# Optimization experiments

Hardware: AMD Instinct MI355X
Metric: run time of the kernel (lower is better)

Reference implementation:

```python
import jax, jax.numpy as jnp
import numpy as np

N_SITES = 100000
DIM = 128
KSIZE = 7  # 7^3 = 343 offsets
GRID = 160


def _build_sparse_structure(seed=0):
    """Sample N_SITES unique voxels in a GRID^3 volume and build the
    depthwise-conv kernel map: neighbor_idx[i, k] = index of site at
    coords[i] + offset[k], or N_SITES (sentinel -> zero row) if absent."""
    rng = np.random.default_rng(seed)
    lin = rng.choice(GRID ** 3, size=N_SITES, replace=False)
    coords = np.stack(np.unravel_index(lin, (GRID, GRID, GRID)), axis=1).astype(np.int64)  # [N,3]
    lookup = np.full(GRID ** 3, N_SITES, dtype=np.int32)
    lookup[lin] = np.arange(N_SITES, dtype=np.int32)
    r = KSIZE // 2
    offs = np.stack(np.meshgrid(*([np.arange(-r, r + 1)] * 3), indexing="ij"), axis=-1).reshape(-1, 3)  # [343,3]
    K = offs.shape[0]
    neighbor_idx = np.full((N_SITES, K), N_SITES, dtype=np.int32)
    for k in range(K):
        nb = coords + offs[k]
        ok = np.all((nb >= 0) & (nb < GRID), axis=1)
        nb_lin = (nb[ok, 0] * GRID + nb[ok, 1]) * GRID + nb[ok, 2]
        neighbor_idx[ok, k] = lookup[nb_lin]
    return neighbor_idx


def setup_inputs() -> dict:
    key = jax.random.key(0)
    ks = jax.random.split(key, 12)
    neighbor_idx = jnp.asarray(_build_sparse_structure(0))
    d, h = DIM, 4 * DIM
    K = KSIZE ** 3
    return {
        "feats": jax.random.normal(ks[0], (N_SITES, d), jnp.float32),
        "neighbor_idx": neighbor_idx,
        "dw_w": jax.random.normal(ks[1], (K, d), jnp.float32) * 0.05,
        "dw_b": jax.random.normal(ks[2], (d,), jnp.float32) * 0.02,
        "ln_g": 1.0 + 0.1 * jax.random.normal(ks[3], (d,), jnp.float32),
        "ln_b": 0.02 * jax.random.normal(ks[4], (d,), jnp.float32),
        "w1": jax.random.normal(ks[5], (d, h), jnp.float32) * (1.0 / np.sqrt(d)),
        "b1": 0.02 * jax.random.normal(ks[6], (h,), jnp.float32),
        "grn_g": 0.1 * jax.random.normal(ks[7], (1, h), jnp.float32),
        "grn_b": 0.02 * jax.random.normal(ks[8], (1, h), jnp.float32),
        "w2": jax.random.normal(ks[9], (h, d), jnp.float32) * (1.0 / np.sqrt(h)),
        "b2": 0.02 * jax.random.normal(ks[10], (d,), jnp.float32),
    }


def reference(feats, neighbor_idx, dw_w, dw_b, ln_g, ln_b, w1, b1, grn_g, grn_b, w2, b2):
    eps = 1e-6
    n, d = feats.shape
    # --- sparse depthwise conv: gather-multiply-accumulate over kernel offsets ---
    f_pad = jnp.concatenate([feats, jnp.zeros((1, d), feats.dtype)], axis=0)  # sentinel row

    def step(acc, xs):
        idx_k, w_k = xs  # idx_k: [N], w_k: [dim]
        return acc + f_pad[idx_k] * w_k, None

    x, _ = jax.lax.scan(step, jnp.zeros_like(feats), (neighbor_idx.T, dw_w))
    x = x + dw_b
    # --- LayerNorm over channels ---
    mu = jnp.mean(x, axis=-1, keepdims=True)
    var = jnp.var(x, axis=-1, keepdims=True)
    x = (x - mu) / jnp.sqrt(var + eps) * ln_g + ln_b
    # --- pwconv1 -> GELU (exact, matching torch default) ---
    x = jax.nn.gelu(x @ w1 + b1, approximate=False)  # [N, 4*dim]
    # --- GRN: L2 norm over all sites (dim=0), per channel ---
    gx = jnp.sqrt(jnp.sum(x * x, axis=0, keepdims=True))  # [1, 4*dim]
    nx = gx / (jnp.mean(gx, axis=-1, keepdims=True) + eps)
    x = grn_g * (x * nx) + grn_b + x
    # --- pwconv2 + residual (drop_path identity in eval) ---
    x = x @ w2 + b2
    return feats + x
```

## Files before the change

### kernel.cpp

```cpp
#include <hip/hip_runtime.h>

typedef unsigned short u16;
typedef unsigned int u32;
typedef __attribute__((ext_vector_type(8))) short bf16x8;
typedef __attribute__((ext_vector_type(4))) float f32x4;

__device__ __forceinline__ u16 f2bf(float f) {
    u32 u = __float_as_uint(f);
    return (u16)((u + 0x7FFFu + ((u >> 16) & 1u)) >> 16);
}
__device__ __forceinline__ int sw_idx(int r, int c) { return r * 16 + (c ^ (r & 15)); }

__device__ __forceinline__ float fast_gelu(float x) {
    const float x3 = x * x * x;
    const float y2 = 1.5957691216057308f * (x + 0.044715f * x3);
    const float u = __expf(fminf(y2, 80.f));
    const float th = (u - 1.f) / (u + 1.f);
    return 0.5f * x * (1.f + th);
}

__global__ __launch_bounds__(256) void cast_feats_k(
    const float* __restrict__ src, u16* __restrict__ dst, int n4)
{
    const int e = blockIdx.x * 256 + threadIdx.x;
    if (e >= n4) return;
    const float4 v = *(const float4*)(src + (size_t)e * 4);
    uint2 o;
    o.x = (u32)f2bf(v.x) | ((u32)f2bf(v.y) << 16);
    o.y = (u32)f2bf(v.z) | ((u32)f2bf(v.w) << 16);
    *(uint2*)(dst + (size_t)e * 4) = o;
}

__global__ __launch_bounds__(256) void dwln_k(
    const u16* __restrict__ featsb, const int* __restrict__ nb,
    const u16* __restrict__ dwwb, const float* __restrict__ dw_b,
    const float* __restrict__ ln_g, const float* __restrict__ ln_b,
    u16* __restrict__ xln, int nsites)
{
    __shared__ int lists[8][348];
    const int w = threadIdx.x >> 6;
    const int lane = threadIdx.x & 63;
    const int s0 = blockIdx.x * 8 + w * 2;
    if (s0 >= nsites) return;
    const bool two = (s0 + 1) < nsites;
    const int* rowA = nb + (size_t)s0 * 343;
    const int* rowB = nb + (size_t)(two ? s0 + 1 : s0) * 343;
    int idxA[6], idxB[6];
    #pragma unroll
    for (int j = 0; j < 5; ++j) {
        idxA[j] = rowA[lane + j * 64];
        const int vb = rowB[lane + j * 64];
        idxB[j] = two ? vb : nsites;
    }
    idxA[5] = (lane < 23) ? rowA[320 + lane] : nsites;
    idxB[5] = (two && lane < 23) ? rowB[320 + lane] : nsites;
    int cA = 0, cB = 0;
    #pragma unroll
    for (int i = 0; i < 6; ++i) {
        cA += (idxA[i] < nsites) ? 1 : 0;
        cB += (idxB[i] < nsites) ? 1 : 0;
    }
    const int packed = cA | (cB << 16);
    int pre = packed;
    #pragma unroll
    for (int off = 1; off < 64; off <<= 1) {
        const int v = __shfl_up(pre, off, 64);
        if (lane >= off) pre += v;
    }
    const int tot = __shfl(pre, 63, 64);
    const int cntA = tot & 0xFFFF, cntB = tot >> 16;
    pre -= packed;
    int pA = pre & 0xFFFF, pB = pre >> 16;
    #pragma unroll
    for (int i = 0; i < 6; ++i) {
        const int k = (i < 5) ? (lane + i * 64) : (320 + lane);
        if (idxA[i] < nsites) lists[w * 2][pA++] = idxA[i] | (k << 17);
        if (idxB[i] < nsites) lists[w * 2 + 1][pB++] = idxB[i] | (k << 17);
    }
    float xA0 = 0.f, xA1 = 0.f, xB0 = 0.f, xB1 = 0.f;
    const int mx = (cntA > cntB) ? cntA : cntB;
    for (int base = 0; base < mx; base += 4) {
        u32 fa[4], wa[4], fb[4], wb[4];
        #pragma unroll
        for (int i = 0; i < 4; ++i) {
            if (base + i < cntA) {
                const int p = lists[w * 2][base + i];
                fa[i] = *(const u32*)(featsb + (size_t)(p & 0x1FFFF) * 128 + lane * 2);
                wa[i] = *(const u32*)(dwwb + (size_t)(p >> 17) * 128 + lane * 2);
            } else { fa[i] = 0u; wa[i] = 0u; }
            if (base + i < cntB) {
                const int p = lists[w * 2 + 1][base + i];
                fb[i] = *(const u32*)(featsb + (size_t)(p & 0x1FFFF) * 128 + lane * 2);
                wb[i] = *(const u32*)(dwwb + (size_t)(p >> 17) * 128 + lane * 2);
            } else { fb[i] = 0u; wb[i] = 0u; }
        }
        #pragma unroll
        for (int i = 0; i < 4; ++i) {
            xA0 += __uint_as_float(fa[i] << 16) * __uint_as_float(wa[i] << 16);
            xA1 += __uint_as_float(fa[i] & 0xFFFF0000u) * __uint_as_float(wa[i] & 0xFFFF0000u);
            xB0 += __uint_as_float(fb[i] << 16) * __uint_as_float(wb[i] << 16);
            xB1 += __uint_as_float(fb[i] & 0xFFFF0000u) * __uint_as_float(wb[i] & 0xFFFF0000u);
        }
    }
    const float2 bv = *(const float2*)(dw_b + lane * 2);
    const float2 gv = *(const float2*)(ln_g + lane * 2);
    const float2 lbv = *(const float2*)(ln_b + lane * 2);
    #pragma unroll
    for (int sidx = 0; sidx < 2; ++sidx) {
        if (sidx == 1 && !two) break;
        float a0 = (sidx == 0) ? xA0 : xB0;
        float a1 = (sidx == 0) ? xA1 : xB1;
        a0 += bv.x; a1 += bv.y;
        float s = a0 + a1, ss = a0 * a0 + a1 * a1;
        #pragma unroll
        for (int off = 32; off > 0; off >>= 1) {
            s += __shfl_xor(s, off, 64);
            ss += __shfl_xor(ss, off, 64);
        }
        const float mean = s * (1.f / 128.f);
        const float var = ss * (1.f / 128.f) - mean * mean;
        const float rstd = rsqrtf(fmaxf(var, 0.f) + 1e-6f);
        const float y0 = (a0 - mean) * rstd * gv.x + lbv.x;
        const float y1 = (a1 - mean) * rstd * gv.y + lbv.y;
        *(u32*)(xln + (size_t)(s0 + sidx) * 128 + lane * 2) =
            (u32)f2bf(y0) | ((u32)f2bf(y1) << 16);
    }
}

__global__ __launch_bounds__(256) void transpose_w1_k(
    const float* __restrict__ w1, u16* __restrict__ w1t)
{
    const int e = blockIdx.x * 256 + threadIdx.x;
    const int n = e >> 7, k = e & 127;
    w1t[e] = f2bf(w1[k * 512 + n]);
}

__global__ __launch_bounds__(256, 4) void gemm1_k(
    const u16* __restrict__ xln, const u16* __restrict__ w1t,
    const float* __restrict__ b1, u16* __restrict__ h,
    float* __restrict__ gx_sq, int nsites)
{
    __shared__ float s_red[128];
    const int t = threadIdx.x;
    const int n0 = blockIdx.x * 128;
    const int m0 = blockIdx.y * 64;
    const int lane = t & 63;
    const int w = t >> 6;
    const int wn = w * 32;
    const int l15 = lane & 15, quad = lane >> 4;
    if (t < 128) s_red[t] = 0.f;
    __syncthreads();
    f32x4 acc[2][4];
    #pragma unroll
    for (int i = 0; i < 2; ++i)
        #pragma unroll
        for (int j = 0; j < 4; ++j) acc[i][j] = f32x4{0.f, 0.f, 0.f, 0.f};
    const u16* a_base = w1t + (size_t)(n0 + wn + l15) * 128 + quad * 8;
    const u16* b_base = xln + (size_t)(m0 + l15) * 128 + quad * 8;
    #pragma unroll
    for (int ks = 0; ks < 4; ++ks) {
        const int koff = ks * 32;
        bf16x8 a[2], b[4];
        #pragma unroll
        for (int nt = 0; nt < 2; ++nt)
            a[nt] = *(const bf16x8*)(a_base + (size_t)nt * 16 * 128 + koff);
        #pragma unroll
        for (int mt = 0; mt < 4; ++mt)
            b[mt] = *(const bf16x8*)(b_base + (size_t)mt * 16 * 128 + koff);
        #pragma unroll
        for (int nt = 0; nt < 2; ++nt)
            #pragma unroll
            for (int mt = 0; mt < 4; ++mt)
                acc[nt][mt] = __builtin_amdgcn_mfma_f32_16x16x32_bf16(a[nt], b[mt], acc[nt][mt], 0, 0, 0);
    }
    float ssl[2][4] = {{0.f,0.f,0.f,0.f},{0.f,0.f,0.f,0.f}};
    #pragma unroll
    for (int nt = 0; nt < 2; ++nt) {
        const int chb = n0 + wn + nt * 16 + quad * 4;
        const float4 b1v = *(const float4*)(b1 + chb);
        #pragma unroll
        for (int mt = 0; mt < 4; ++mt) {
            const int site = m0 + mt * 16 + l15;
            if (site < nsites) {
                float v[4];
                #pragma unroll
                for (int rg = 0; rg < 4; ++rg) {
                    v[rg] = fast_gelu(acc[nt][mt][rg] + ((const float*)&b1v)[rg]);
                    ssl[nt][rg] += v[rg] * v[rg];
                }
                uint2 o;
                o.x = (u32)f2bf(v[0]) | ((u32)f2bf(v[1]) << 16);
                o.y = (u32)f2bf(v[2]) | ((u32)f2bf(v[3]) << 16);
                *(uint2*)(h + (size_t)site * 512 + chb) = o;
            }
        }
    }
    #pragma unroll
    for (int nt = 0; nt < 2; ++nt)
        #pragma unroll
        for (int rg = 0; rg < 4; ++rg) {
            float v = ssl[nt][rg];
            v += __shfl_xor(v, 1, 64);
            v += __shfl_xor(v, 2, 64);
            v += __shfl_xor(v, 4, 64);
            v += __shfl_xor(v, 8, 64);
            if (l15 == 0) atomicAdd(&s_red[wn + nt * 16 + quad * 4 + rg], v);
        }
    __syncthreads();
    if (t < 128) atomicAdd(&gx_sq[n0 + t], s_red[t]);
}

__global__ __launch_bounds__(512) void grn_scale_k(
    const float* __restrict__ gx_sq, const float* __restrict__ grn_g,
    const float* __restrict__ grn_b, const float* __restrict__ w2,
    const float* __restrict__ b2, float* __restrict__ scale, float* __restrict__ b_eff)
{
    __shared__ float red[512];
    __shared__ float redb[512];
    const int t = threadIdx.x;
    const float g = sqrtf(gx_sq[t]);
    red[t] = g;
    __syncthreads();
    #pragma unroll
    for (int off = 256; off > 0; off >>= 1) {
        if (t < off) red[t] += red[t + off];
        __syncthreads();
    }
    const float mean = red[0] * (1.f / 512.f);
    scale[t] = grn_g[t] * (g / (mean + 1e-6f)) + 1.f;
    const int dc = t & 127, grp = t >> 7;
    float p = 0.f;
    #pragma unroll 8
    for (int i = 0; i < 128; ++i) {
        const int c = grp * 128 + i;
        p += grn_b[c] * w2[(size_t)c * 128 + dc];
    }
    redb[t] = p;
    __syncthreads();
    if (t < 128) b_eff[t] = b2[t] + redb[t] + redb[t + 128] + redb[t + 256] + redb[t + 384];
}

__global__ __launch_bounds__(256) void w2t_k(
    const float* __restrict__ scale, const float* __restrict__ w2,
    u16* __restrict__ w2t)
{
    const int e = blockIdx.x * 256 + threadIdx.x;
    const int c = e & 511, dc = e >> 9;
    w2t[e] = f2bf(scale[c] * w2[(size_t)c * 128 + dc]);
}

__global__ __launch_bounds__(256, 4) void gemm2_k(
    const u16* __restrict__ h, const u16* __restrict__ w2t,
    const float* __restrict__ b_eff, const float* __restrict__ feats,
    float* __restrict__ out, int nsites)
{
    const int t = threadIdx.x;
    const int m0 = blockIdx.x * 64;
    const int lane = t & 63;
    const int w = t >> 6;
    const int wn = w * 32;
    const int l15 = lane & 15, quad = lane >> 4;
    f32x4 acc[4][2];
    #pragma unroll
    for (int i = 0; i < 4; ++i)
        #pragma unroll
        for (int j = 0; j < 2; ++j) acc[i][j] = f32x4{0.f, 0.f, 0.f, 0.f};
    const u16* a_base = h + (size_t)(m0 + l15) * 512 + quad * 8;
    const u16* b_base = w2t + (size_t)(wn + l15) * 512 + quad * 8;
    #pragma unroll
    for (int ks = 0; ks < 16; ++ks) {
        const int koff = ks * 32;
        bf16x8 a[4], b[2];
        #pragma unroll
        for (int mt = 0; mt < 4; ++mt)
            a[mt] = *(const bf16x8*)(a_base + (size_t)mt * 16 * 512 + koff);
        #pragma unroll
        for (int nt = 0; nt < 2; ++nt)
            b[nt] = *(const bf16x8*)(b_base + (size_t)nt * 16 * 512 + koff);
        #pragma unroll
        for (int mt = 0; mt < 4; ++mt)
            #pragma unroll
            for (int nt = 0; nt < 2; ++nt)
                acc[mt][nt] = __builtin_amdgcn_mfma_f32_16x16x32_bf16(a[mt], b[nt], acc[mt][nt], 0, 0, 0);
    }
    float be[2]; int col[2];
    #pragma unroll
    for (int nt = 0; nt < 2; ++nt) {
        col[nt] = wn + nt * 16 + l15;
        be[nt] = b_eff[col[nt]];
    }
    #pragma unroll
    for (int mt = 0; mt < 4; ++mt) {
        const int rbase = m0 + mt * 16 + quad * 4;
        #pragma unroll
        for (int nt = 0; nt < 2; ++nt) {
            #pragma unroll
            for (int rg = 0; rg < 4; ++rg) {
                const int rowg = rbase + rg;
                if (rowg < nsites) {
                    out[(size_t)rowg * 128 + col[nt]] =
                        acc[mt][nt][rg] + be[nt] + feats[(size_t)rowg * 128 + col[nt]];
                }
            }
        }
    }
}

extern "C" void kernel_launch(void* const* d_in, const int* in_sizes, int n_in,
                              void* d_out, int out_size, void* d_ws, size_t ws_size,
                              hipStream_t stream) {
    const float* feats = (const float*)d_in[0];
    const int* nb      = (const int*)d_in[1];
    const float* dw_w  = (const float*)d_in[2];
    const float* dw_b  = (const float*)d_in[3];
    const float* ln_g  = (const float*)d_in[4];
    const float* ln_b  = (const float*)d_in[5];
    const float* w1    = (const float*)d_in[6];
    const float* b1    = (const float*)d_in[7];
    const float* grn_g = (const float*)d_in[8];
    const float* grn_b = (const float*)d_in[9];
    const float* w2    = (const float*)d_in[10];
    const float* b2    = (const float*)d_in[11];
    float* out = (float*)d_out;
    const int nsites = in_sizes[0] / 128;

    char* ws = (char*)d_ws;
    size_t off = 0;
    u16* xln   = (u16*)(ws + off);  off += (((size_t)(nsites + 128) * 128 * 2) + 255) & ~(size_t)255;
    u16* h     = (u16*)(ws + off);  off += (((size_t)(nsites + 128) * 512 * 2) + 255) & ~(size_t)255;
    u16* featsb= (u16*)(ws + off);  off += (((size_t)nsites * 128 * 2) + 255) & ~(size_t)255;
    u16* dwwb  = (u16*)(ws + off);  off += 343 * 128 * 2 + 128;
    u16* w1t   = (u16*)(ws + off);  off += 512 * 128 * 2;
    u16* w2t   = (u16*)(ws + off);  off += 128 * 512 * 2;
    float* gx_sq = (float*)(ws + off); off += 512 * 4;
    float* scale = (float*)(ws + off); off += 512 * 4;
    float* b_eff = (float*)(ws + off); off += 128 * 4;

    hipMemsetAsync(gx_sq, 0, 512 * sizeof(float), stream);
    const int nfeat4 = nsites * 32;
    cast_feats_k<<<(nfeat4 + 255) / 256, 256, 0, stream>>>(feats, featsb, nfeat4);
    const int ndww4 = 343 * 32;
    cast_feats_k<<<(ndww4 + 255) / 256, 256, 0, stream>>>(dw_w, dwwb, ndww4);
    transpose_w1_k<<<256, 256, 0, stream>>>(w1, w1t);
    dwln_k<<<(nsites + 7) / 8, 256, 0, stream>>>(featsb, nb, dwwb, dw_b, ln_g, ln_b, xln, nsites);
    const int m1blocks = (nsites + 63) / 64;
    gemm1_k<<<dim3(4, m1blocks), 256, 0, stream>>>(xln, w1t, b1, h, gx_sq, nsites);
    grn_scale_k<<<1, 512, 0, stream>>>(gx_sq, grn_g, grn_b, w2, b2, scale, b_eff);
    w2t_k<<<256, 256, 0, stream>>>(scale, w2, w2t);
    const int m2blocks = (nsites + 63) / 64;
    gemm2_k<<<m2blocks, 256, 0, stream>>>(h, w2t, b_eff, feats, out, nsites);
}
```

Baseline: 491.0 us.

## Prefetch next K-slice in GEMMs, vectorize gemm2 epilogue, split b_eff reduction

Both MFMA GEMM kernels now double-buffer their register operands, loading the next K-slice before issuing the current MFMAs so global-load latency overlaps compute. gemm2 swaps its operand roles so each lane owns four consecutive output channels, which lets the epilogue read feats and write out with float4 accesses instead of scalar ones. The grn_b·w2 bias reduction moves out of the single-block GRN kernel into a separate 8-block kernel that uses atomics and runs before the conv. This shortens the serial tail between the GEMMs, at the cost of an extra memset, atomics and more register pressure.

```diff
diff --git a/kernel.cpp b/kernel.cpp
--- a/kernel.cpp
+++ b/kernel.cpp
@@ -9,7 +9,6 @@
     u32 u = __float_as_uint(f);
     return (u16)((u + 0x7FFFu + ((u >> 16) & 1u)) >> 16);
 }
-__device__ __forceinline__ int sw_idx(int r, int c) { return r * 16 + (c ^ (r & 15)); }
 
 __device__ __forceinline__ float fast_gelu(float x) {
     const float x3 = x * x * x;
@@ -157,21 +156,33 @@
         for (int j = 0; j < 4; ++j) acc[i][j] = f32x4{0.f, 0.f, 0.f, 0.f};
     const u16* a_base = w1t + (size_t)(n0 + wn + l15) * 128 + quad * 8;
     const u16* b_base = xln + (size_t)(m0 + l15) * 128 + quad * 8;
+    bf16x8 aC[2], bC[4], aN[2], bN[4];
+    #pragma unroll
+    for (int nt = 0; nt < 2; ++nt) aC[nt] = *(const bf16x8*)(a_base + (size_t)nt * 16 * 128);
+    #pragma unroll
+    for (int mt = 0; mt < 4; ++mt) bC[mt] = *(const bf16x8*)(b_base + (size_t)mt * 16 * 128);
     #pragma unroll
     for (int ks = 0; ks < 4; ++ks) {
-        const int koff = ks * 32;
-        bf16x8 a[2], b[4];
+        if (ks < 3) {
+            const int koff = (ks + 1) * 32;
+            #pragma unroll
+            for (int nt = 0; nt < 2; ++nt)
+                aN[nt] = *(const bf16x8*)(a_base + (size_t)nt * 16 * 128 + koff);
+            #pragma unroll
+            for (int mt = 0; mt < 4; ++mt)
+                bN[mt] = *(const bf16x8*)(b_base + (size_t)mt * 16 * 128 + koff);
+        }
         #pragma unroll
         for (int nt = 0; nt < 2; ++nt)
-            a[nt] = *(const bf16x8*)(a_base + (size_t)nt * 16 * 128 + koff);
-        #pragma unroll
-        for (int mt = 0; mt < 4; ++mt)
-            b[mt] = *(const bf16x8*)(b_base + (size_t)mt * 16 * 128 + koff);
-        #pragma unroll
-        for (int nt = 0; nt < 2; ++nt)
             #pragma unroll
             for (int mt = 0; mt < 4; ++mt)
-                acc[nt][mt] = __builtin_amdgcn_mfma_f32_16x16x32_bf16(a[nt], b[mt], acc[nt][mt], 0, 0, 0);
+                acc[nt][mt] = __builtin_amdgcn_mfma_f32_16x16x32_bf16(aC[nt], bC[mt], acc[nt][mt], 0, 0, 0);
+        if (ks < 3) {
+            #pragma unroll
+            for (int nt = 0; nt < 2; ++nt) aC[nt] = aN[nt];
+            #pragma unroll
+            for (int mt = 0; mt < 4; ++mt) bC[mt] = bN[mt];
+        }
     }
     float ssl[2][4] = {{0.f,0.f,0.f,0.f},{0.f,0.f,0.f,0.f}};
     #pragma unroll
@@ -210,13 +221,30 @@
     if (t < 128) atomicAdd(&gx_sq[n0 + t], s_red[t]);
 }
 
+__global__ __launch_bounds__(256) void beff_k(
+    const float* __restrict__ grn_b, const float* __restrict__ w2,
+    float* __restrict__ b_eff)
+{
+    __shared__ float red[256];
+    const int t = threadIdx.x;
+    const int dc = t & 127, part = t >> 7;
+    const int c0 = blockIdx.x * 64 + part * 32;
+    float p = 0.f;
+    #pragma unroll 8
+    for (int i = 0; i < 32; ++i) {
+        const int c = c0 + i;
+        p += grn_b[c] * w2[(size_t)c * 128 + dc];
+    }
+    red[t] = p;
+    __syncthreads();
+    if (t < 128) atomicAdd(&b_eff[t], red[t] + red[t + 128]);
+}
+
 __global__ __launch_bounds__(512) void grn_scale_k(
     const float* __restrict__ gx_sq, const float* __restrict__ grn_g,
-    const float* __restrict__ grn_b, const float* __restrict__ w2,
-    const float* __restrict__ b2, float* __restrict__ scale, float* __restrict__ b_eff)
+    float* __restrict__ scale)
 {
     __shared__ float red[512];
-    __shared__ float redb[512];
     const int t = threadIdx.x;
     const float g = sqrtf(gx_sq[t]);
     red[t] = g;
@@ -228,16 +256,6 @@
     }
     const float mean = red[0] * (1.f / 512.f);
     scale[t] = grn_g[t] * (g / (mean + 1e-6f)) + 1.f;
-    const int dc = t & 127, grp = t >> 7;
-    float p = 0.f;
-    #pragma unroll 8
-    for (int i = 0; i < 128; ++i) {
-        const int c = grp * 128 + i;
-        p += grn_b[c] * w2[(size_t)c * 128 + dc];
-    }
-    redb[t] = p;
-    __syncthreads();
-    if (t < 128) b_eff[t] = b2[t] + redb[t] + redb[t + 128] + redb[t + 256] + redb[t + 384];
 }
 
 __global__ __launch_bounds__(256) void w2t_k(
@@ -251,7 +269,8 @@
 
 __global__ __launch_bounds__(256, 4) void gemm2_k(
     const u16* __restrict__ h, const u16* __restrict__ w2t,
-    const float* __restrict__ b_eff, const float* __restrict__ feats,
+    const float* __restrict__ b_eff, const float* __restrict__ b2,
+    const float* __restrict__ feats,
     float* __restrict__ out, int nsites)
 {
     const int t = threadIdx.x;
@@ -260,47 +279,57 @@
     const int w = t >> 6;
     const int wn = w * 32;
     const int l15 = lane & 15, quad = lane >> 4;
-    f32x4 acc[4][2];
-    #pragma unroll
-    for (int i = 0; i < 4; ++i)
-        #pragma unroll
-        for (int j = 0; j < 2; ++j) acc[i][j] = f32x4{0.f, 0.f, 0.f, 0.f};
-    const u16* a_base = h + (size_t)(m0 + l15) * 512 + quad * 8;
-    const u16* b_base = w2t + (size_t)(wn + l15) * 512 + quad * 8;
+    f32x4 acc[2][4];
+    #pragma unroll
+    for (int i = 0; i < 2; ++i)
+        #pragma unroll
+        for (int j = 0; j < 4; ++j) acc[i][j] = f32x4{0.f, 0.f, 0.f, 0.f};
+    const u16* a_base = w2t + (size_t)(wn + l15) * 512 + quad * 8;
+    const u16* b_base = h + (size_t)(m0 + l15) * 512 + quad * 8;
+    bf16x8 aC[2], bC[4], aN[2], bN[4];
+    #pragma unroll
+    for (int nt = 0; nt < 2; ++nt) aC[nt] = *(const bf16x8*)(a_base + (size_t)nt * 16 * 512);
+    #pragma unroll
+    for (int mt = 0; mt < 4; ++mt) bC[mt] = *(const bf16x8*)(b_base + (size_t)mt * 16 * 512);
     #pragma unroll
     for (int ks = 0; ks < 16; ++ks) {
-        const int koff = ks * 32;
-        bf16x8 a[4], b[2];
-        #pragma unroll
-        for (int mt = 0; mt < 4; ++mt)
-            a[mt] = *(const bf16x8*)(a_base + (size_t)mt * 16 * 512 + koff);
+        if (ks < 15) {
+            const int koff = (ks + 1) * 32;
+            #pragma unroll
+            for (int nt = 0; nt < 2; ++nt)
+                aN[nt] = *(const bf16x8*)(a_base + (size_t)nt * 16 * 512 + koff);
+            #pragma unroll
+            for (int mt = 0; mt < 4; ++mt)
+                bN[mt] = *(const bf16x8*)(b_base + (size_t)mt * 16 * 512 + koff);
+        }
         #pragma unroll
         for (int nt = 0; nt < 2; ++nt)
-            b[nt] = *(const bf16x8*)(b_base + (size_t)nt * 16 * 512 + koff);
-        #pragma unroll
-        for (int mt = 0; mt < 4; ++mt)
-            #pragma unroll
-            for (int nt = 0; nt < 2; ++nt)
-                acc[mt][nt] = __builtin_amdgcn_mfma_f32_16x16x32_bf16(a[mt], b[nt], acc[mt][nt], 0, 0, 0);
-    }
-    float be[2]; int col[2];
+            #pragma unroll
+            for (int mt = 0; mt < 4; ++mt)
+                acc[nt][mt] = __builtin_amdgcn_mfma_f32_16x16x32_bf16(aC[nt], bC[mt], acc[nt][mt], 0, 0, 0);
+        if (ks < 15) {
+            #pragma unroll
+            for (int nt = 0; nt < 2; ++nt) aC[nt] = aN[nt];
+            #pragma unroll
+            for (int mt = 0; mt < 4; ++mt) bC[mt] = bN[mt];
+        }
+    }
     #pragma unroll
     for (int nt = 0; nt < 2; ++nt) {
-        col[nt] = wn + nt * 16 + l15;
-        be[nt] = b_eff[col[nt]];
-    }
-    #pragma unroll
-    for (int mt = 0; mt < 4; ++mt) {
-        const int rbase = m0 + mt * 16 + quad * 4;
-        #pragma unroll
-        for (int nt = 0; nt < 2; ++nt) {
-            #pragma unroll
-            for (int rg = 0; rg < 4; ++rg) {
-                const int rowg = rbase + rg;
-                if (rowg < nsites) {
-                    out[(size_t)rowg * 128 + col[nt]] =
-                        acc[mt][nt][rg] + be[nt] + feats[(size_t)rowg * 128 + col[nt]];
-                }
+        const int chb = wn + nt * 16 + quad * 4;
+        const float4 bev = *(const float4*)(b_eff + chb);
+        const float4 b2v = *(const float4*)(b2 + chb);
+        #pragma unroll
+        for (int mt = 0; mt < 4; ++mt) {
+            const int site = m0 + mt * 16 + l15;
+            if (site < nsites) {
+                const float4 fv = *(const float4*)(feats + (size_t)site * 128 + chb);
+                float4 o;
+                o.x = acc[nt][mt][0] + bev.x + b2v.x + fv.x;
+                o.y = acc[nt][mt][1] + bev.y + b2v.y + fv.y;
+                o.z = acc[nt][mt][2] + bev.z + b2v.z + fv.z;
+                o.w = acc[nt][mt][3] + bev.w + b2v.w + fv.w;
+                *(float4*)(out + (size_t)site * 128 + chb) = o;
             }
         }
     }
@@ -337,16 +366,18 @@
     float* b_eff = (float*)(ws + off); off += 128 * 4;
 
     hipMemsetAsync(gx_sq, 0, 512 * sizeof(float), stream);
+    hipMemsetAsync(b_eff, 0, 128 * sizeof(float), stream);
     const int nfeat4 = nsites * 32;
     cast_feats_k<<<(nfeat4 + 255) / 256, 256, 0, stream>>>(feats, featsb, nfeat4);
     const int ndww4 = 343 * 32;
     cast_feats_k<<<(ndww4 + 255) / 256, 256, 0, stream>>>(dw_w, dwwb, ndww4);
     transpose_w1_k<<<256, 256, 0, stream>>>(w1, w1t);
+    beff_k<<<8, 256, 0, stream>>>(grn_b, w2, b_eff);
     dwln_k<<<(nsites + 7) / 8, 256, 0, stream>>>(featsb, nb, dwwb, dw_b, ln_g, ln_b, xln, nsites);
     const int m1blocks = (nsites + 63) / 64;
     gemm1_k<<<dim3(4, m1blocks), 256, 0, stream>>>(xln, w1t, b1, h, gx_sq, nsites);
-    grn_scale_k<<<1, 512, 0, stream>>>(gx_sq, grn_g, grn_b, w2, b2, scale, b_eff);
+    grn_scale_k<<<1, 512, 0, stream>>>(gx_sq, grn_g, scale);
     w2t_k<<<256, 256, 0, stream>>>(scale, w2, w2t);
     const int m2blocks = (nsites + 63) / 64;
-    gemm2_k<<<m2blocks, 256, 0, stream>>>(h, w2t, b_eff, feats, out, nsites);
-}
+    gemm2_k<<<m2blocks, 256, 0, stream>>>(h, w2t, b_eff, b2, feats, out, nsites);
+}
```

Result: faster. 473.2 us (-3.6%).
